# Kernel tuning notes

Measured on AMD Instinct MI355X. Metric: run time of the kernel, lower is better.

## Reference

```python
import jax, jax.numpy as jnp
import numpy as np

T, B, IN, H1, H2, OUT = 1024, 512, 20, 128, 64, 3

def _uniform(key, shape, bound):
    return jax.random.uniform(key, shape, jnp.float32, -bound, bound)

def setup_inputs() -> dict:
    key = jax.random.key(0)
    ks = jax.random.split(key, 11)
    b1 = 1.0 / np.sqrt(H1)
    b2 = 1.0 / np.sqrt(H2)
    return {
        "x": jax.random.normal(ks[0], (T, B, IN), jnp.float32),
        "W_ih0": _uniform(ks[1], (4 * H1, IN), b1),
        "W_hh0": _uniform(ks[2], (4 * H1, H1), b1),
        "b_ih0": _uniform(ks[3], (4 * H1,), b1),
        "b_hh0": _uniform(ks[4], (4 * H1,), b1),
        "W_ih1": _uniform(ks[5], (4 * H2, H1), b2),
        "W_hh1": _uniform(ks[6], (4 * H2, H2), b2),
        "b_ih1": _uniform(ks[7], (4 * H2,), b2),
        "b_hh1": _uniform(ks[8], (4 * H2,), b2),
        "W_d": _uniform(ks[9], (OUT, H2), b2),
        "b_d": _uniform(ks[10], (OUT,), b2),
    }

def _lstm_layer(x, W_ih, W_hh, b_ih, b_hh, hidden):
    # x: (T, B, in_dim); PyTorch gate order: i, f, g, o
    batch = x.shape[1]
    x_proj = jnp.einsum("tbi,gi->tbg", x, W_ih) + (b_ih + b_hh)  # (T,B,4H)

    def step(carry, xp):
        h, c = carry
        gates = xp + h @ W_hh.T  # (B,4H)
        i, f, g, o = jnp.split(gates, 4, axis=-1)
        i = jax.nn.sigmoid(i)
        f = jax.nn.sigmoid(f)
        g = jnp.tanh(g)
        o = jax.nn.sigmoid(o)
        c = f * c + i * g
        h = o * jnp.tanh(c)
        return (h, c), h

    h0 = jnp.zeros((batch, hidden), x.dtype)
    c0 = jnp.zeros((batch, hidden), x.dtype)
    _, ys = jax.lax.scan(step, (h0, c0), x_proj)
    return ys  # (T, B, H)

def reference(x, W_ih0, W_hh0, b_ih0, b_hh0, W_ih1, W_hh1, b_ih1, b_hh1, W_d, b_d):
    h1 = _lstm_layer(x, W_ih0, W_hh0, b_ih0, b_hh0, H1)   # (T,B,128)
    h2 = _lstm_layer(h1, W_ih1, W_hh1, b_ih1, b_hh1, H2)  # (T,B,64)
    # Faithful to original: lstm_out[:, -1, :] in seq-first layout picks the
    # last batch element at every timestep -> (T, 64)
    last = h2[:, -1, :]
    act = jax.nn.relu(last)
    # Dropout in eval mode is identity.
    return act @ W_d.T + b_d  # (T, 3)
```

## Files before the change

### kernel.cpp

```cpp
#include <hip/hip_runtime.h>
#include <hip/hip_bf16.h>


#define T_STEPS 1024
#define BATCH   512
#define IN_F    20
#define H1_     128
#define H2_     64
#define OUT_F   3
#define G1_     (4*H1_)
#define G2_     (4*H2_)

typedef float f4 __attribute__((ext_vector_type(4)));

__device__ __forceinline__ float sigmoidf_(float x) {
    return 1.0f / (1.0f + __expf(-x));
}
__device__ __forceinline__ float tanhf_(float x) {
    return 1.0f - 2.0f / (__expf(2.0f * x) + 1.0f);
}

#define REP16(M) M(0) M(1) M(2) M(3) M(4) M(5) M(6) M(7) \
                 M(8) M(9) M(10) M(11) M(12) M(13) M(14) M(15)

#define ASM_LOAD_16Q(PTR)                                                     \
    asm volatile(                                                             \
        "global_load_dwordx4 %0,  %16, off\n\t"                              \
        "global_load_dwordx4 %1,  %16, off offset:16\n\t"                    \
        "global_load_dwordx4 %2,  %16, off offset:32\n\t"                    \
        "global_load_dwordx4 %3,  %16, off offset:48\n\t"                    \
        "global_load_dwordx4 %4,  %16, off offset:64\n\t"                    \
        "global_load_dwordx4 %5,  %16, off offset:80\n\t"                    \
        "global_load_dwordx4 %6,  %16, off offset:96\n\t"                    \
        "global_load_dwordx4 %7,  %16, off offset:112\n\t"                   \
        "global_load_dwordx4 %8,  %16, off offset:128\n\t"                   \
        "global_load_dwordx4 %9,  %16, off offset:144\n\t"                   \
        "global_load_dwordx4 %10, %16, off offset:160\n\t"                   \
        "global_load_dwordx4 %11, %16, off offset:176\n\t"                   \
        "global_load_dwordx4 %12, %16, off offset:192\n\t"                   \
        "global_load_dwordx4 %13, %16, off offset:208\n\t"                   \
        "global_load_dwordx4 %14, %16, off offset:224\n\t"                   \
        "global_load_dwordx4 %15, %16, off offset:240\n\t"                   \
        "s_waitcnt vmcnt(0)"                                                  \
        : "=&v"(w_0), "=&v"(w_1), "=&v"(w_2), "=&v"(w_3),                    \
          "=&v"(w_4), "=&v"(w_5), "=&v"(w_6), "=&v"(w_7),                    \
          "=&v"(w_8), "=&v"(w_9), "=&v"(w_10), "=&v"(w_11),                  \
          "=&v"(w_12), "=&v"(w_13), "=&v"(w_14), "=&v"(w_15)                 \
        : "v"(PTR))

__global__ void xproj_kernel(const float* __restrict__ x,
                             const float* __restrict__ W_ih0,
                             const float* __restrict__ b_ih0,
                             const float* __restrict__ b_hh0,
                             float* __restrict__ xp1)
{
    const int t = blockIdx.x;
    const int g = threadIdx.x;
    const float* xr = x + ((size_t)t * BATCH + (BATCH - 1)) * IN_F;
    const float* w  = W_ih0 + g * IN_F;
    float acc = b_ih0[g] + b_hh0[g];
#pragma unroll
    for (int i = 0; i < IN_F; ++i) acc = fmaf(xr[i], w[i], acc);
    xp1[t * G1_ + g] = acc;
}

__global__ __attribute__((amdgpu_flat_work_group_size(1024, 1024),
                          amdgpu_waves_per_eu(4, 4)))
void lstm1_kernel(const float* __restrict__ xp1,
                  const float* __restrict__ W_hh0,
                  float* __restrict__ h1seq)
{
    const int tid = threadIdx.x;
    const int g   = tid & 511;
    const int hf  = tid >> 9;

    __shared__ f4    sh1[H1_ / 4];
    __shared__ float sp1[G1_ * 3];

    const f4* pw = (const f4*)(W_hh0 + (size_t)g * H1_ + hf * 64);
    f4 w_0, w_1, w_2, w_3, w_4, w_5, w_6, w_7,
       w_8, w_9, w_10, w_11, w_12, w_13, w_14, w_15;
    ASM_LOAD_16Q(pw);

    if (tid < H1_ / 4) sh1[tid] = f4{0.f, 0.f, 0.f, 0.f};
    float c1 = 0.0f;
    __syncthreads();

    const f4* hb = sh1 + hf * 16;
    float xp_cur = (hf == 0) ? xp1[g] : 0.0f;

    for (int t = 0; t < T_STEPS; ++t) {
        float xp_next = 0.0f;
        {
            const int tn = (t + 1 < T_STEPS) ? (t + 1) : (T_STEPS - 1);
            if (hf == 0) xp_next = xp1[(size_t)tn * G1_ + g];
        }

        float ax = 0.f, ay = 0.f, az = 0.f, aw = 0.f;
#define P1S(k) { const f4 h4 = hb[k];                                        \
        ax = fmaf(w_##k.x, h4.x, ax); ay = fmaf(w_##k.y, h4.y, ay);          \
        az = fmaf(w_##k.z, h4.z, az); aw = fmaf(w_##k.w, h4.w, aw); }
        REP16(P1S)
#undef P1S
        sp1[g * 3 + hf] = ((ax + ay) + (az + aw)) + xp_cur;
        __syncthreads();

        if (tid < H1_) {
            const float vi = sp1[tid * 3]         + sp1[tid * 3 + 1];
            const float vf = sp1[(H1_   + tid)*3] + sp1[(H1_   + tid)*3 + 1];
            const float vg = sp1[(2*H1_ + tid)*3] + sp1[(2*H1_ + tid)*3 + 1];
            const float vo = sp1[(3*H1_ + tid)*3] + sp1[(3*H1_ + tid)*3 + 1];
            c1 = fmaf(sigmoidf_(vf), c1, sigmoidf_(vi) * tanhf_(vg));
            const float h = sigmoidf_(vo) * tanhf_(c1);
            ((float*)sh1)[tid] = h;
            h1seq[(size_t)t * H1_ + tid] = h;
        }
        __syncthreads();
        xp_cur = xp_next;
    }
}

__global__ void xproj2_kernel(const float* __restrict__ h1seq,
                              const float* __restrict__ W_ih1,
                              const float* __restrict__ b_ih1,
                              const float* __restrict__ b_hh1,
                              float* __restrict__ xp2)
{
    const int t = blockIdx.x;
    const int g = threadIdx.x;
    __shared__ f4 sh[H1_ / 4];
    if (g < H1_ / 4) sh[g] = ((const f4*)(h1seq + (size_t)t * H1_))[g];
    __syncthreads();
    const f4* w = (const f4*)(W_ih1 + (size_t)g * H1_);
    float ax = 0.f, ay = 0.f, az = 0.f, aw = 0.f;
#pragma unroll
    for (int k = 0; k < H1_ / 4; ++k) {
        const f4 h4 = sh[k]; const f4 w4 = w[k];
        ax = fmaf(w4.x, h4.x, ax); ay = fmaf(w4.y, h4.y, ay);
        az = fmaf(w4.z, h4.z, az); aw = fmaf(w4.w, h4.w, aw);
    }
    xp2[(size_t)t * G2_ + g] = ((ax + ay) + (az + aw)) + b_ih1[g] + b_hh1[g];
}

__global__ __attribute__((amdgpu_flat_work_group_size(256, 256),
                          amdgpu_waves_per_eu(1, 1)))
void lstm2_kernel(const float* __restrict__ xp2,
                  const float* __restrict__ W_hh1,
                  float* __restrict__ h2seq)
{
    const int tid = threadIdx.x;

    __shared__ f4    sh2[H2_ / 4];
    __shared__ float sg2[G2_];

    const f4* pw = (const f4*)(W_hh1 + (size_t)tid * H2_);
    f4 w_0, w_1, w_2, w_3, w_4, w_5, w_6, w_7,
       w_8, w_9, w_10, w_11, w_12, w_13, w_14, w_15;
    ASM_LOAD_16Q(pw);

    if (tid < H2_ / 4) sh2[tid] = f4{0.f, 0.f, 0.f, 0.f};
    float c2 = 0.0f;
    __syncthreads();

    float xp_cur = xp2[tid];

    for (int t = 0; t < T_STEPS; ++t) {
        float xp_next;
        {
            const int tn = (t + 1 < T_STEPS) ? (t + 1) : (T_STEPS - 1);
            xp_next = xp2[(size_t)tn * G2_ + tid];
        }

        float ax = 0.f, ay = 0.f, az = 0.f, aw = 0.f;
#define P1S(k) { const f4 h4 = sh2[k];                                       \
        ax = fmaf(w_##k.x, h4.x, ax); ay = fmaf(w_##k.y, h4.y, ay);          \
        az = fmaf(w_##k.z, h4.z, az); aw = fmaf(w_##k.w, h4.w, aw); }
        REP16(P1S)
#undef P1S
        sg2[tid] = ((ax + ay) + (az + aw)) + xp_cur;
        __syncthreads();

        if (tid < H2_) {
            const float vi = sg2[tid];
            const float vf = sg2[H2_ + tid];
            const float vg = sg2[2 * H2_ + tid];
            const float vo = sg2[3 * H2_ + tid];
            c2 = fmaf(sigmoidf_(vf), c2, sigmoidf_(vi) * tanhf_(vg));
            const float h = sigmoidf_(vo) * tanhf_(c2);
            ((float*)sh2)[tid] = h;
            h2seq[(size_t)t * H2_ + tid] = h;
        }
        __syncthreads();
        xp_cur = xp_next;
    }
}

__global__ void head_kernel(const float* __restrict__ h2seq,
                            const float* __restrict__ W_d,
                            const float* __restrict__ b_d,
                            float* __restrict__ out)
{
    const int idx = blockIdx.x * blockDim.x + threadIdx.x;
    if (idx >= T_STEPS * OUT_F) return;
    const int t = idx / OUT_F;
    const int o = idx - t * OUT_F;
    const float* hr = h2seq + (size_t)t * H2_;
    const float* w  = W_d + o * H2_;
    float acc = b_d[o];
#pragma unroll
    for (int j = 0; j < H2_; ++j) acc = fmaf(fmaxf(hr[j], 0.0f), w[j], acc);
    out[idx] = acc;
}

extern "C" void kernel_launch(void* const* d_in, const int* in_sizes, int n_in,
                              void* d_out, int out_size, void* d_ws, size_t ws_size,
                              hipStream_t stream) {
    const float* x     = (const float*)d_in[0];
    const float* W_ih0 = (const float*)d_in[1];
    const float* W_hh0 = (const float*)d_in[2];
    const float* b_ih0 = (const float*)d_in[3];
    const float* b_hh0 = (const float*)d_in[4];
    const float* W_ih1 = (const float*)d_in[5];
    const float* W_hh1 = (const float*)d_in[6];
    const float* b_ih1 = (const float*)d_in[7];
    const float* b_hh1 = (const float*)d_in[8];
    const float* W_d   = (const float*)d_in[9];
    const float* b_d   = (const float*)d_in[10];

    float* out   = (float*)d_out;
    float* xp1   = (float*)d_ws;
    float* h1seq = xp1 + (size_t)T_STEPS * G1_;
    float* h2seq = h1seq + (size_t)T_STEPS * H1_;
    float* xp2   = xp1;

    hipLaunchKernelGGL(xproj_kernel, dim3(T_STEPS), dim3(G1_), 0, stream,
                       x, W_ih0, b_ih0, b_hh0, xp1);
    hipLaunchKernelGGL(lstm1_kernel, dim3(1), dim3(1024), 0, stream,
                       xp1, W_hh0, h1seq);
    hipLaunchKernelGGL(xproj2_kernel, dim3(T_STEPS), dim3(G2_), 0, stream,
                       h1seq, W_ih1, b_ih1, b_hh1, xp2);
    hipLaunchKernelGGL(lstm2_kernel, dim3(1), dim3(512 / 2), 0, stream,
                       xp2, W_hh1, h2seq);
    hipLaunchKernelGGL(head_kernel, dim3((T_STEPS * OUT_F + 255) / 256), dim3(256),
                       0, stream, h2seq, W_d, b_d, out);
}
```

Measured before the change: 1.581 ms.

## Run layer-1 recurrent matvec on MFMA with split-fp16 weights in AGPRs

New measurement: 1.864 ms. 17.9% more time.

```diff
diff --git a/kernel.cpp b/kernel.cpp
--- a/kernel.cpp
+++ b/kernel.cpp
@@ -12,12 +12,17 @@
 #define G2_     (4*H2_)
 
 typedef float f4 __attribute__((ext_vector_type(4)));
+typedef _Float16 h8 __attribute__((ext_vector_type(8)));
+typedef unsigned int u32;
 
 __device__ __forceinline__ float sigmoidf_(float x) {
     return 1.0f / (1.0f + __expf(-x));
 }
 __device__ __forceinline__ float tanhf_(float x) {
     return 1.0f - 2.0f / (__expf(2.0f * x) + 1.0f);
+}
+__device__ __forceinline__ u32 pkh(_Float16 a, _Float16 b) {
+    union { _Float16 h[2]; u32 u; } cv; cv.h[0] = a; cv.h[1] = b; return cv.u;
 }
 
 #define REP16(M) M(0) M(1) M(2) M(3) M(4) M(5) M(6) M(7) \
@@ -48,6 +53,29 @@
           "=&v"(w_12), "=&v"(w_13), "=&v"(w_14), "=&v"(w_15)                 \
         : "v"(PTR))
 
+#define PIN1(R, V) asm volatile("v_accvgpr_write_b32 " R ", %0" :: "v"((u32)(V)) : R)
+
+#define MF(ACC, AR, B) \
+    asm volatile("v_mfma_f32_16x16x32_f16 %0, " AR ", %1, %0" : "+v"(ACC) : "v"(B))
+
+#define FRAG(M, KT, R0,R1,R2,R3,R4,R5,R6,R7) do {                             \
+    const float* wp_ = W_hh0 + (size_t)(64*w + 16*(M) + lr) * H1_             \
+                       + (KT)*32 + kq*8;                                      \
+    f4 xa_ = *(const f4*)wp_; f4 xb_ = *(const f4*)(wp_ + 4);                 \
+    _Float16 h0_=(_Float16)xa_.x, h1_=(_Float16)xa_.y,                        \
+             h2_=(_Float16)xa_.z, h3_=(_Float16)xa_.w,                        \
+             h4_=(_Float16)xb_.x, h5_=(_Float16)xb_.y,                        \
+             h6_=(_Float16)xb_.z, h7_=(_Float16)xb_.w;                        \
+    _Float16 l0_=(_Float16)(xa_.x-(float)h0_), l1_=(_Float16)(xa_.y-(float)h1_),\
+             l2_=(_Float16)(xa_.z-(float)h2_), l3_=(_Float16)(xa_.w-(float)h3_),\
+             l4_=(_Float16)(xb_.x-(float)h4_), l5_=(_Float16)(xb_.y-(float)h5_),\
+             l6_=(_Float16)(xb_.z-(float)h6_), l7_=(_Float16)(xb_.w-(float)h7_);\
+    PIN1(R0, pkh(h0_,h1_)); PIN1(R1, pkh(h2_,h3_));                           \
+    PIN1(R2, pkh(h4_,h5_)); PIN1(R3, pkh(h6_,h7_));                           \
+    PIN1(R4, pkh(l0_,l1_)); PIN1(R5, pkh(l2_,l3_));                           \
+    PIN1(R6, pkh(l4_,l5_)); PIN1(R7, pkh(l6_,l7_));                           \
+} while (0)
+
 __global__ void xproj_kernel(const float* __restrict__ x,
                              const float* __restrict__ W_ih0,
                              const float* __restrict__ b_ih0,
@@ -64,59 +92,108 @@
     xp1[t * G1_ + g] = acc;
 }
 
-__global__ __attribute__((amdgpu_flat_work_group_size(1024, 1024),
-                          amdgpu_waves_per_eu(4, 4)))
+__global__ __attribute__((amdgpu_flat_work_group_size(512, 512),
+                          amdgpu_waves_per_eu(2, 2)))
 void lstm1_kernel(const float* __restrict__ xp1,
                   const float* __restrict__ W_hh0,
                   float* __restrict__ h1seq)
 {
     const int tid = threadIdx.x;
-    const int g   = tid & 511;
-    const int hf  = tid >> 9;
-
-    __shared__ f4    sh1[H1_ / 4];
-    __shared__ float sp1[G1_ * 3];
-
-    const f4* pw = (const f4*)(W_hh0 + (size_t)g * H1_ + hf * 64);
-    f4 w_0, w_1, w_2, w_3, w_4, w_5, w_6, w_7,
-       w_8, w_9, w_10, w_11, w_12, w_13, w_14, w_15;
-    ASM_LOAD_16Q(pw);
-
-    if (tid < H1_ / 4) sh1[tid] = f4{0.f, 0.f, 0.f, 0.f};
+    const int w   = tid >> 6;
+    const int l   = tid & 63;
+    const int lr  = l & 15;
+    const int kq  = l >> 4;
+
+    __shared__ float sg[G1_];
+    __shared__ h8    sh_hi8[16];
+    __shared__ h8    sh_lo8[16];
+
+    FRAG(0,0,"a0","a1","a2","a3","a4","a5","a6","a7");
+    FRAG(0,1,"a8","a9","a10","a11","a12","a13","a14","a15");
+    FRAG(0,2,"a16","a17","a18","a19","a20","a21","a22","a23");
+    FRAG(0,3,"a24","a25","a26","a27","a28","a29","a30","a31");
+    FRAG(1,0,"a32","a33","a34","a35","a36","a37","a38","a39");
+    FRAG(1,1,"a40","a41","a42","a43","a44","a45","a46","a47");
+    FRAG(1,2,"a48","a49","a50","a51","a52","a53","a54","a55");
+    FRAG(1,3,"a56","a57","a58","a59","a60","a61","a62","a63");
+    FRAG(2,0,"a64","a65","a66","a67","a68","a69","a70","a71");
+    FRAG(2,1,"a72","a73","a74","a75","a76","a77","a78","a79");
+    FRAG(2,2,"a80","a81","a82","a83","a84","a85","a86","a87");
+    FRAG(2,3,"a88","a89","a90","a91","a92","a93","a94","a95");
+    FRAG(3,0,"a96","a97","a98","a99","a100","a101","a102","a103");
+    FRAG(3,1,"a104","a105","a106","a107","a108","a109","a110","a111");
+    FRAG(3,2,"a112","a113","a114","a115","a116","a117","a118","a119");
+    FRAG(3,3,"a120","a121","a122","a123","a124","a125","a126","a127");
+
+    if (tid < 16) { sh_hi8[tid] = (h8)0; sh_lo8[tid] = (h8)0; }
     float c1 = 0.0f;
     __syncthreads();
 
-    const f4* hb = sh1 + hf * 16;
-    float xp_cur = (hf == 0) ? xp1[g] : 0.0f;
+    const float* xb = xp1 + 64 * w + kq * 4;
+    f4 xq0 = *(const f4*)(xb);
+    f4 xq1 = *(const f4*)(xb + 16);
+    f4 xq2 = *(const f4*)(xb + 32);
+    f4 xq3 = *(const f4*)(xb + 48);
 
     for (int t = 0; t < T_STEPS; ++t) {
-        float xp_next = 0.0f;
+        const h8 bh0 = sh_hi8[kq],      bl0 = sh_lo8[kq];
+        const h8 bh1 = sh_hi8[4 + kq],  bl1 = sh_lo8[4 + kq];
+        const h8 bh2 = sh_hi8[8 + kq],  bl2 = sh_lo8[8 + kq];
+        const h8 bh3 = sh_hi8[12 + kq], bl3 = sh_lo8[12 + kq];
+
+        f4 ac0 = xq0, ac1 = xq1, ac2 = xq2, ac3 = xq3;
         {
             const int tn = (t + 1 < T_STEPS) ? (t + 1) : (T_STEPS - 1);
-            if (hf == 0) xp_next = xp1[(size_t)tn * G1_ + g];
-        }
-
-        float ax = 0.f, ay = 0.f, az = 0.f, aw = 0.f;
-#define P1S(k) { const f4 h4 = hb[k];                                        \
-        ax = fmaf(w_##k.x, h4.x, ax); ay = fmaf(w_##k.y, h4.y, ay);          \
-        az = fmaf(w_##k.z, h4.z, az); aw = fmaf(w_##k.w, h4.w, aw); }
-        REP16(P1S)
-#undef P1S
-        sp1[g * 3 + hf] = ((ax + ay) + (az + aw)) + xp_cur;
+            const float* xn = xb + (size_t)tn * G1_;
+            xq0 = *(const f4*)(xn);
+            xq1 = *(const f4*)(xn + 16);
+            xq2 = *(const f4*)(xn + 32);
+            xq3 = *(const f4*)(xn + 48);
+        }
+        asm volatile("s_nop 3" : "+v"(ac0), "+v"(ac1), "+v"(ac2), "+v"(ac3));
+
+        MF(ac0,"a[0:3]",bh0);   MF(ac1,"a[32:35]",bh0);  MF(ac2,"a[64:67]",bh0);  MF(ac3,"a[96:99]",bh0);
+        MF(ac0,"a[0:3]",bl0);   MF(ac1,"a[32:35]",bl0);  MF(ac2,"a[64:67]",bl0);  MF(ac3,"a[96:99]",bl0);
+        MF(ac0,"a[4:7]",bh0);   MF(ac1,"a[36:39]",bh0);  MF(ac2,"a[68:71]",bh0);  MF(ac3,"a[100:103]",bh0);
+
+        MF(ac0,"a[8:11]",bh1);  MF(ac1,"a[40:43]",bh1);  MF(ac2,"a[72:75]",bh1);  MF(ac3,"a[104:107]",bh1);
+        MF(ac0,"a[8:11]",bl1);  MF(ac1,"a[40:43]",bl1);  MF(ac2,"a[72:75]",bl1);  MF(ac3,"a[104:107]",bl1);
+        MF(ac0,"a[12:15]",bh1); MF(ac1,"a[44:47]",bh1);  MF(ac2,"a[76:79]",bh1);  MF(ac3,"a[108:111]",bh1);
+
+        MF(ac0,"a[16:19]",bh2); MF(ac1,"a[48:51]",bh2);  MF(ac2,"a[80:83]",bh2);  MF(ac3,"a[112:115]",bh2);
+        MF(ac0,"a[16:19]",bl2); MF(ac1,"a[48:51]",bl2);  MF(ac2,"a[80:83]",bl2);  MF(ac3,"a[112:115]",bl2);
+        MF(ac0,"a[20:23]",bh2); MF(ac1,"a[52:55]",bh2);  MF(ac2,"a[84:87]",bh2);  MF(ac3,"a[116:119]",bh2);
+
+        MF(ac0,"a[24:27]",bh3); MF(ac1,"a[56:59]",bh3);  MF(ac2,"a[88:91]",bh3);  MF(ac3,"a[120:123]",bh3);
+        MF(ac0,"a[24:27]",bl3); MF(ac1,"a[56:59]",bl3);  MF(ac2,"a[88:91]",bl3);  MF(ac3,"a[120:123]",bl3);
+        MF(ac0,"a[28:31]",bh3); MF(ac1,"a[60:63]",bh3);  MF(ac2,"a[92:95]",bh3);  MF(ac3,"a[124:127]",bh3);
+
+        asm volatile("s_nop 7\n\ts_nop 7"
+                     : "+v"(ac0), "+v"(ac1), "+v"(ac2), "+v"(ac3));
+
+        if (lr == 0) {
+            f4* sg4 = (f4*)sg;
+            sg4[16 * w + 0 + kq] = ac0;
+            sg4[16 * w + 4 + kq] = ac1;
+            sg4[16 * w + 8 + kq] = ac2;
+            sg4[16 * w + 12 + kq] = ac3;
+        }
         __syncthreads();
 
         if (tid < H1_) {
-            const float vi = sp1[tid * 3]         + sp1[tid * 3 + 1];
-            const float vf = sp1[(H1_   + tid)*3] + sp1[(H1_   + tid)*3 + 1];
-            const float vg = sp1[(2*H1_ + tid)*3] + sp1[(2*H1_ + tid)*3 + 1];
-            const float vo = sp1[(3*H1_ + tid)*3] + sp1[(3*H1_ + tid)*3 + 1];
+            const float vi = sg[tid];
+            const float vf = sg[H1_ + tid];
+            const float vg = sg[2 * H1_ + tid];
+            const float vo = sg[3 * H1_ + tid];
             c1 = fmaf(sigmoidf_(vf), c1, sigmoidf_(vi) * tanhf_(vg));
             const float h = sigmoidf_(vo) * tanhf_(c1);
-            ((float*)sh1)[tid] = h;
+            const _Float16 hh = (_Float16)h;
+            const _Float16 hl = (_Float16)(h - (float)hh);
+            ((_Float16*)sh_hi8)[tid] = hh;
+            ((_Float16*)sh_lo8)[tid] = hl;
             h1seq[(size_t)t * H1_ + tid] = h;
         }
         __syncthreads();
-        xp_cur = xp_next;
     }
 }
 
@@ -235,11 +312,11 @@
 
     hipLaunchKernelGGL(xproj_kernel, dim3(T_STEPS), dim3(G1_), 0, stream,
                        x, W_ih0, b_ih0, b_hh0, xp1);
-    hipLaunchKernelGGL(lstm1_kernel, dim3(1), dim3(1024), 0, stream,
+    hipLaunchKernelGGL(lstm1_kernel, dim3(1), dim3(512), 0, stream,
                        xp1, W_hh0, h1seq);
     hipLaunchKernelGGL(xproj2_kernel, dim3(T_STEPS), dim3(G2_), 0, stream,
                        h1seq, W_ih1, b_ih1, b_hh1, xp2);
-    hipLaunchKernelGGL(lstm2_kernel, dim3(1), dim3(512 / 2), 0, stream,
+    hipLaunchKernelGGL(lstm2_kernel, dim3(1), dim3(256), 0, stream,
                        xp2, W_hh1, h2seq);
     hipLaunchKernelGGL(head_kernel, dim3((T_STEPS * OUT_F + 255) / 256), dim3(256),
                        0, stream, h2seq, W_d, b_d, out);
```

## Use fp16 dot2 with split-precision hidden state in LSTM recurrences

Applied to the files above, without the earlier changes.

Result: slower. 1.962 ms (+24.1%).

```diff
diff --git a/kernel.cpp b/kernel.cpp
--- a/kernel.cpp
+++ b/kernel.cpp
@@ -12,6 +12,9 @@
 #define G2_     (4*H2_)
 
 typedef float f4 __attribute__((ext_vector_type(4)));
+typedef unsigned int u32;
+typedef u32 u4 __attribute__((ext_vector_type(4)));
+typedef _Float16 h2 __attribute__((ext_vector_type(2)));
 
 __device__ __forceinline__ float sigmoidf_(float x) {
     return 1.0f / (1.0f + __expf(-x));
@@ -19,34 +22,22 @@
 __device__ __forceinline__ float tanhf_(float x) {
     return 1.0f - 2.0f / (__expf(2.0f * x) + 1.0f);
 }
-
-#define REP16(M) M(0) M(1) M(2) M(3) M(4) M(5) M(6) M(7) \
-                 M(8) M(9) M(10) M(11) M(12) M(13) M(14) M(15)
-
-#define ASM_LOAD_16Q(PTR)                                                     \
-    asm volatile(                                                             \
-        "global_load_dwordx4 %0,  %16, off\n\t"                              \
-        "global_load_dwordx4 %1,  %16, off offset:16\n\t"                    \
-        "global_load_dwordx4 %2,  %16, off offset:32\n\t"                    \
-        "global_load_dwordx4 %3,  %16, off offset:48\n\t"                    \
-        "global_load_dwordx4 %4,  %16, off offset:64\n\t"                    \
-        "global_load_dwordx4 %5,  %16, off offset:80\n\t"                    \
-        "global_load_dwordx4 %6,  %16, off offset:96\n\t"                    \
-        "global_load_dwordx4 %7,  %16, off offset:112\n\t"                   \
-        "global_load_dwordx4 %8,  %16, off offset:128\n\t"                   \
-        "global_load_dwordx4 %9,  %16, off offset:144\n\t"                   \
-        "global_load_dwordx4 %10, %16, off offset:160\n\t"                   \
-        "global_load_dwordx4 %11, %16, off offset:176\n\t"                   \
-        "global_load_dwordx4 %12, %16, off offset:192\n\t"                   \
-        "global_load_dwordx4 %13, %16, off offset:208\n\t"                   \
-        "global_load_dwordx4 %14, %16, off offset:224\n\t"                   \
-        "global_load_dwordx4 %15, %16, off offset:240\n\t"                   \
-        "s_waitcnt vmcnt(0)"                                                  \
-        : "=&v"(w_0), "=&v"(w_1), "=&v"(w_2), "=&v"(w_3),                    \
-          "=&v"(w_4), "=&v"(w_5), "=&v"(w_6), "=&v"(w_7),                    \
-          "=&v"(w_8), "=&v"(w_9), "=&v"(w_10), "=&v"(w_11),                  \
-          "=&v"(w_12), "=&v"(w_13), "=&v"(w_14), "=&v"(w_15)                 \
-        : "v"(PTR))
+__device__ __forceinline__ h2 as_h2(u32 v) {
+    union { u32 u; h2 h; } c; c.u = v; return c.h;
+}
+__device__ __forceinline__ u32 pkh(float a, float b) {
+    union { _Float16 h[2]; u32 u; } c;
+    c.h[0] = (_Float16)a; c.h[1] = (_Float16)b; return c.u;
+}
+__device__ __forceinline__ float fdot2_(h2 a, h2 b, float c) {
+#if __has_builtin(__builtin_amdgcn_fdot2)
+    return __builtin_amdgcn_fdot2(a, b, c, false);
+#else
+    float d = c;
+    asm("v_dot2_f32_f16 %0, %1, %2, %0" : "+v"(d) : "v"(a), "v"(b));
+    return d;
+#endif
+}
 
 __global__ void xproj_kernel(const float* __restrict__ x,
                              const float* __restrict__ W_ih0,
@@ -64,55 +55,76 @@
     xp1[t * G1_ + g] = acc;
 }
 
-__global__ __attribute__((amdgpu_flat_work_group_size(1024, 1024),
-                          amdgpu_waves_per_eu(4, 4)))
+__global__ __attribute__((amdgpu_flat_work_group_size(512, 512),
+                          amdgpu_waves_per_eu(2, 2)))
 void lstm1_kernel(const float* __restrict__ xp1,
                   const float* __restrict__ W_hh0,
                   float* __restrict__ h1seq)
 {
     const int tid = threadIdx.x;
-    const int g   = tid & 511;
-    const int hf  = tid >> 9;
-
-    __shared__ f4    sh1[H1_ / 4];
-    __shared__ float sp1[G1_ * 3];
-
-    const f4* pw = (const f4*)(W_hh0 + (size_t)g * H1_ + hf * 64);
-    f4 w_0, w_1, w_2, w_3, w_4, w_5, w_6, w_7,
-       w_8, w_9, w_10, w_11, w_12, w_13, w_14, w_15;
-    ASM_LOAD_16Q(pw);
-
-    if (tid < H1_ / 4) sh1[tid] = f4{0.f, 0.f, 0.f, 0.f};
+
+    __shared__ u4    swW[512 * 17];
+    __shared__ u4    shhi[16];
+    __shared__ u4    shlo[16];
+    __shared__ float sg[G1_];
+
+    {
+        const float* wr = W_hh0 + (size_t)tid * H1_;
+#pragma unroll
+        for (int j = 0; j < 16; ++j) {
+            const f4 lo = *(const f4*)(wr + j * 8);
+            const f4 hi = *(const f4*)(wr + j * 8 + 4);
+            u4 pk;
+            pk.x = pkh(lo.x, lo.y);
+            pk.y = pkh(lo.z, lo.w);
+            pk.z = pkh(hi.x, hi.y);
+            pk.w = pkh(hi.z, hi.w);
+            swW[tid * 17 + j] = pk;
+        }
+    }
+    if (tid < 16) { shhi[tid] = u4{0,0,0,0}; shlo[tid] = u4{0,0,0,0}; }
     float c1 = 0.0f;
     __syncthreads();
 
-    const f4* hb = sh1 + hf * 16;
-    float xp_cur = (hf == 0) ? xp1[g] : 0.0f;
+    const u4* wrow = swW + tid * 17;
+    float xp_cur = xp1[tid];
 
     for (int t = 0; t < T_STEPS; ++t) {
-        float xp_next = 0.0f;
+        float xp_next;
         {
             const int tn = (t + 1 < T_STEPS) ? (t + 1) : (T_STEPS - 1);
-            if (hf == 0) xp_next = xp1[(size_t)tn * G1_ + g];
-        }
-
-        float ax = 0.f, ay = 0.f, az = 0.f, aw = 0.f;
-#define P1S(k) { const f4 h4 = hb[k];                                        \
-        ax = fmaf(w_##k.x, h4.x, ax); ay = fmaf(w_##k.y, h4.y, ay);          \
-        az = fmaf(w_##k.z, h4.z, az); aw = fmaf(w_##k.w, h4.w, aw); }
-        REP16(P1S)
-#undef P1S
-        sp1[g * 3 + hf] = ((ax + ay) + (az + aw)) + xp_cur;
+            xp_next = xp1[(size_t)tn * G1_ + tid];
+        }
+
+        float a0 = 0.f, a1 = 0.f, a2 = 0.f, a3 = 0.f;
+#pragma unroll
+        for (int j = 0; j < 16; ++j) {
+            const u4 wq = wrow[j];
+            const u4 hh = shhi[j];
+            const u4 hl = shlo[j];
+            a0 = fdot2_(as_h2(wq.x), as_h2(hh.x), a0);
+            a1 = fdot2_(as_h2(wq.y), as_h2(hh.y), a1);
+            a0 = fdot2_(as_h2(wq.z), as_h2(hh.z), a0);
+            a1 = fdot2_(as_h2(wq.w), as_h2(hh.w), a1);
+            a2 = fdot2_(as_h2(wq.x), as_h2(hl.x), a2);
+            a3 = fdot2_(as_h2(wq.y), as_h2(hl.y), a3);
+            a2 = fdot2_(as_h2(wq.z), as_h2(hl.z), a2);
+            a3 = fdot2_(as_h2(wq.w), as_h2(hl.w), a3);
+        }
+        sg[tid] = ((a0 + a1) + 0.000244140625f * (a2 + a3)) + xp_cur;
         __syncthreads();
 
         if (tid < H1_) {
-            const float vi = sp1[tid * 3]         + sp1[tid * 3 + 1];
-            const float vf = sp1[(H1_   + tid)*3] + sp1[(H1_   + tid)*3 + 1];
-            const float vg = sp1[(2*H1_ + tid)*3] + sp1[(2*H1_ + tid)*3 + 1];
-            const float vo = sp1[(3*H1_ + tid)*3] + sp1[(3*H1_ + tid)*3 + 1];
+            const float vi = sg[tid];
+            const float vf = sg[H1_ + tid];
+            const float vg = sg[2 * H1_ + tid];
+            const float vo = sg[3 * H1_ + tid];
             c1 = fmaf(sigmoidf_(vf), c1, sigmoidf_(vi) * tanhf_(vg));
             const float h = sigmoidf_(vo) * tanhf_(c1);
-            ((float*)sh1)[tid] = h;
+            const _Float16 hh16 = (_Float16)h;
+            const float hrem = (h - (float)hh16) * 4096.0f;
+            ((_Float16*)shhi)[tid] = hh16;
+            ((_Float16*)shlo)[tid] = (_Float16)hrem;
             h1seq[(size_t)t * H1_ + tid] = h;
         }
         __syncthreads();
@@ -150,18 +162,30 @@
 {
     const int tid = threadIdx.x;
 
-    __shared__ f4    sh2[H2_ / 4];
+    __shared__ u4    swW2[256 * 9];
+    __shared__ u4    shhi[8];
+    __shared__ u4    shlo[8];
     __shared__ float sg2[G2_];
 
-    const f4* pw = (const f4*)(W_hh1 + (size_t)tid * H2_);
-    f4 w_0, w_1, w_2, w_3, w_4, w_5, w_6, w_7,
-       w_8, w_9, w_10, w_11, w_12, w_13, w_14, w_15;
-    ASM_LOAD_16Q(pw);
-
-    if (tid < H2_ / 4) sh2[tid] = f4{0.f, 0.f, 0.f, 0.f};
+    {
+        const float* wr = W_hh1 + (size_t)tid * H2_;
+#pragma unroll
+        for (int j = 0; j < 8; ++j) {
+            const f4 lo = *(const f4*)(wr + j * 8);
+            const f4 hi = *(const f4*)(wr + j * 8 + 4);
+            u4 pk;
+            pk.x = pkh(lo.x, lo.y);
+            pk.y = pkh(lo.z, lo.w);
+            pk.z = pkh(hi.x, hi.y);
+            pk.w = pkh(hi.z, hi.w);
+            swW2[tid * 9 + j] = pk;
+        }
+    }
+    if (tid < 8) { shhi[tid] = u4{0,0,0,0}; shlo[tid] = u4{0,0,0,0}; }
     float c2 = 0.0f;
     __syncthreads();
 
+    const u4* wrow = swW2 + tid * 9;
     float xp_cur = xp2[tid];
 
     for (int t = 0; t < T_STEPS; ++t) {
@@ -171,13 +195,22 @@
             xp_next = xp2[(size_t)tn * G2_ + tid];
         }
 
-        float ax = 0.f, ay = 0.f, az = 0.f, aw = 0.f;
-#define P1S(k) { const f4 h4 = sh2[k];                                       \
-        ax = fmaf(w_##k.x, h4.x, ax); ay = fmaf(w_##k.y, h4.y, ay);          \
-        az = fmaf(w_##k.z, h4.z, az); aw = fmaf(w_##k.w, h4.w, aw); }
-        REP16(P1S)
-#undef P1S
-        sg2[tid] = ((ax + ay) + (az + aw)) + xp_cur;
+        float a0 = 0.f, a1 = 0.f, a2 = 0.f, a3 = 0.f;
+#pragma unroll
+        for (int j = 0; j < 8; ++j) {
+            const u4 wq = wrow[j];
+            const u4 hh = shhi[j];
+            const u4 hl = shlo[j];
+            a0 = fdot2_(as_h2(wq.x), as_h2(hh.x), a0);
+            a1 = fdot2_(as_h2(wq.y), as_h2(hh.y), a1);
+            a0 = fdot2_(as_h2(wq.z), as_h2(hh.z), a0);
+            a1 = fdot2_(as_h2(wq.w), as_h2(hh.w), a1);
+            a2 = fdot2_(as_h2(wq.x), as_h2(hl.x), a2);
+            a3 = fdot2_(as_h2(wq.y), as_h2(hl.y), a3);
+            a2 = fdot2_(as_h2(wq.z), as_h2(hl.z), a2);
+            a3 = fdot2_(as_h2(wq.w), as_h2(hl.w), a3);
+        }
+        sg2[tid] = ((a0 + a1) + 0.000244140625f * (a2 + a3)) + xp_cur;
         __syncthreads();
 
         if (tid < H2_) {
@@ -187,7 +220,10 @@
             const float vo = sg2[3 * H2_ + tid];
             c2 = fmaf(sigmoidf_(vf), c2, sigmoidf_(vi) * tanhf_(vg));
             const float h = sigmoidf_(vo) * tanhf_(c2);
-            ((float*)sh2)[tid] = h;
+            const _Float16 hh16 = (_Float16)h;
+            const float hrem = (h - (float)hh16) * 4096.0f;
+            ((_Float16*)shhi)[tid] = hh16;
+            ((_Float16*)shlo)[tid] = (_Float16)hrem;
             h2seq[(size_t)t * H2_ + tid] = h;
         }
         __syncthreads();
@@ -235,11 +271,11 @@
 
     hipLaunchKernelGGL(xproj_kernel, dim3(T_STEPS), dim3(G1_), 0, stream,
                        x, W_ih0, b_ih0, b_hh0, xp1);
-    hipLaunchKernelGGL(lstm1_kernel, dim3(1), dim3(1024), 0, stream,
+    hipLaunchKernelGGL(lstm1_kernel, dim3(1), dim3(512), 0, stream,
                        xp1, W_hh0, h1seq);
     hipLaunchKernelGGL(xproj2_kernel, dim3(T_STEPS), dim3(G2_), 0, stream,
                        h1seq, W_ih1, b_ih1, b_hh1, xp2);
-    hipLaunchKernelGGL(lstm2_kernel, dim3(1), dim3(512 / 2), 0, stream,
+    hipLaunchKernelGGL(lstm2_kernel, dim3(1), dim3(256), 0, stream,
                        xp2, W_hh1, h2seq);
     hipLaunchKernelGGL(head_kernel, dim3((T_STEPS * OUT_F + 255) / 256), dim3(256),
                        0, stream, h2seq, W_d, b_d, out);
```
